# Kernel optimization log

Hardware: AMD Instinct MI355X
Metric: run time of the kernel (lower is better)

Reference implementation:

```python
import jax, jax.numpy as jnp
import numpy as np


def setup_inputs() -> dict:
    key = jax.random.key(0)
    k1, k2 = jax.random.split(key)
    inputs = jax.random.normal(k1, (16, 4096, 512), dtype=jnp.float32)
    # torch init is uniform(-1/num_codes, 1/num_codes); match scale
    codebooks = jax.random.uniform(k2, (4, 1024, 512), dtype=jnp.float32,
                                   minval=-1.0 / 1024, maxval=1.0 / 1024)
    return {"inputs": inputs, "codebooks": codebooks}


def _vq_level(flat, codebook):
    # flat: [N, D], codebook: [K, D]
    dists = (jnp.sum(flat * flat, axis=1, keepdims=True)
             + jnp.sum(codebook * codebook, axis=1)
             - 2.0 * jnp.matmul(flat, codebook.T))  # [N, K]
    idx = jnp.argmin(dists, axis=1)                  # [N]
    quantized = codebook[idx]                         # [N, D]
    return quantized, idx


def reference(inputs, codebooks):
    sg = jax.lax.stop_gradient
    num_levels = codebooks.shape[0]
    shp = inputs.shape
    D = shp[-1]
    flat_in = inputs.reshape(-1, D)

    residual = flat_in
    total_q = jnp.zeros_like(flat_in)
    all_idx = []
    total_q_loss = jnp.float32(0.0)
    total_e_loss = jnp.float32(0.0)
    for lvl in range(num_levels):
        quantized, idx = _vq_level(residual, codebooks[lvl])
        q_loss = jnp.mean((quantized - sg(residual)) ** 2)
        e_loss = jnp.mean((sg(quantized) - residual) ** 2)
        all_idx.append(idx.reshape(shp[:-1]))
        total_q = total_q + quantized
        total_q_loss = total_q_loss + q_loss
        total_e_loss = total_e_loss + e_loss
        residual = residual - sg(quantized)

    total_q = total_q.reshape(shp)
    final_ste = inputs + sg(total_q - inputs)
    return (final_ste,
            total_q_loss / num_levels,
            total_e_loss / num_levels,
            jnp.stack(all_idx, axis=0))
```

## Files before the change

### kernel.cpp

```cpp
#include <hip/hip_runtime.h>


#define NROWS 65536
#define DDIM  512
#define KC    1024

#define AS1 __attribute__((address_space(1)))
#define AS3 __attribute__((address_space(3)))

typedef __attribute__((ext_vector_type(8))) short short8v;
typedef __attribute__((ext_vector_type(4))) float f32x4;

__device__ __forceinline__ unsigned short f2bf(float f) {
  unsigned u = __float_as_uint(f);
  unsigned r = (u + 0x7FFFu + ((u >> 16) & 1u)) >> 16;
  return (unsigned short)r;
}

__device__ __forceinline__ bool lexlt(float v1, int i1, float v2, int i2) {
  return (v1 < v2) || (v1 == v2 && i1 < i2);
}

__device__ __forceinline__ void merge3(float& v0, float& v1, float& v2,
                                       float m0, float m1, float m2) {
  float x1 = fmaxf(v0, m0); v0 = fminf(v0, m0);
  float y = fminf(v1, m1), z = fmaxf(v1, m1);
  float nv1 = fminf(x1, y);
  v2 = fminf(fmaxf(x1, y), fminf(z, fminf(v2, m2)));
  v1 = nv1;
}

__device__ __forceinline__ void top3of4(float k0, float k1, float k2, float k3,
                                        float& m0, float& m1, float& m2) {
  float a = fminf(k0, k1), b = fmaxf(k0, k1);
  float c = fminf(k2, k3), d = fmaxf(k2, k3);
  m0 = fminf(a, c);
  float f = fmaxf(a, c), g = fminf(b, d);
  m1 = fminf(f, g); m2 = fmaxf(f, g);
}

__device__ __forceinline__ void wg_barrier() {
  asm volatile("" ::: "memory");
  __builtin_amdgcn_s_barrier();
  asm volatile("" ::: "memory");
}


__global__ void cnorm_kernel(const float* __restrict__ cbs,
                             float* __restrict__ cn32) {
  const int code = blockIdx.x;
  const int l = threadIdx.x;
  if (l >= 32) return;
  const int b = l >> 3, j = l & 7;
  const float* p = cbs + (size_t)code * DDIM + b * 128 + j;
  float racc;
  {
    #pragma clang fp contract(off)
    float x0 = p[0];
    racc = x0 * x0;
    for (int s = 1; s < 16; ++s) { float x = p[8 * s]; float sq = x * x; racc = racc + sq; }
  }
  {
    #pragma clang fp contract(off)
    float o;
    o = __shfl_xor(racc, 1, 64);  racc = racc + o;
    o = __shfl_xor(racc, 2, 64);  racc = racc + o;
    o = __shfl_xor(racc, 4, 64);  racc = racc + o;
    o = __shfl_xor(racc, 8, 64);  racc = racc + o;
    o = __shfl_xor(racc, 16, 64); racc = racc + o;
    if (l == 0) cn32[code] = racc;
  }
}

__global__ void cvt_bf16_kernel(const float4* __restrict__ in4,
                                ushort4* __restrict__ o4, long n4) {
  for (long i = blockIdx.x * (long)blockDim.x + threadIdx.x; i < n4;
       i += (long)gridDim.x * blockDim.x) {
    float4 v = in4[i];
    ushort4 o; o.x = f2bf(v.x); o.y = f2bf(v.y); o.z = f2bf(v.z); o.w = f2bf(v.w);
    o4[i] = o;
  }
}

__global__ void __launch_bounds__(256)
resupd_kernel(const float4* __restrict__ x4, const float* __restrict__ cbs,
              const float* __restrict__ idx_f, ushort4* __restrict__ res4,
              int nlev) {
  const int gwave = (blockIdx.x * 256 + threadIdx.x) >> 6;
  const int lane  = threadIdx.x & 63;
  const int nwaves = gridDim.x * 4;
  const float4* cb4 = (const float4*)cbs;
  for (int row = gwave; row < NROWS; row += nwaves) {
    int ci[4];
    for (int l = 0; l < nlev; ++l) ci[l] = (int)idx_f[(size_t)l * NROWS + row];
    #pragma unroll
    for (int half = 0; half < 2; ++half) {
      const int p = half * 64 + lane;
      float4 v = x4[(size_t)row * 128 + p];
      for (int l = 0; l < nlev; ++l) {
        const float4 c = cb4[((size_t)(l * KC + ci[l])) * 128 + p];
        v.x -= c.x; v.y -= c.y; v.z -= c.z; v.w -= c.w;
      }
      ushort4 o; o.x = f2bf(v.x); o.y = f2bf(v.y); o.z = f2bf(v.z); o.w = f2bf(v.w);
      res4[(size_t)row * 128 + p] = o;
    }
  }
}

template <int LVL>
__global__ void __launch_bounds__(256, 4)
score_gemm(const ushort* __restrict__ res, const ushort* __restrict__ cbb,
           const float* __restrict__ cn32, float* __restrict__ partials) {
  __shared__ ushort At[2][128 * 32];
  __shared__ ushort Bt[2][128 * 32];
  __shared__ float halfTop[2][2][64][3];

  const int t = threadIdx.x;
  const int w = t >> 6, lane = t & 63;
  const int fr = lane & 15, kg = lane >> 4;
  const int rh = w >> 1, ch = w & 1;
  const int xcd = blockIdx.x & 7;
  const int j   = blockIdx.x >> 3;
  const int colTile = j & 7;
  const int rowTile = xcd * 64 + (j >> 3);
  const int row0 = rowTile * 128;

  const ushort* Asrc = res + (size_t)row0 * DDIM;
  const ushort* Bsrc = cbb + ((size_t)LVL * KC + colTile * 128) * DDIM;

  const int r0s = t >> 2, kq = t & 3;
  const int r1s = 64 + r0s;
  const int swz = (t >> 3) & 3;
  const size_t off0 = (size_t)r0s * DDIM + (size_t)((kq ^ swz) * 8);
  const size_t off1 = (size_t)r1s * DDIM + (size_t)((kq ^ swz) * 8);
  const int kgs = (kg ^ ((fr >> 1) & 3)) * 8;

  f32x4 acc[4][4];
  #pragma unroll
  for (int ri = 0; ri < 4; ++ri)
    #pragma unroll
    for (int ci = 0; ci < 4; ++ci) { f32x4 z = {0.f, 0.f, 0.f, 0.f}; acc[ri][ci] = z; }

#define STG(KS, BI)                                                           \
  do {                                                                        \
    __builtin_amdgcn_global_load_lds(                                         \
        (const AS1 unsigned*)(Asrc + off0 + (KS) * 32),                       \
        (AS3 unsigned*)&At[BI][w * 512], 16, 0, 0);                           \
    __builtin_amdgcn_global_load_lds(                                         \
        (const AS1 unsigned*)(Asrc + off1 + (KS) * 32),                       \
        (AS3 unsigned*)&At[BI][2048 + w * 512], 16, 0, 0);                    \
    __builtin_amdgcn_global_load_lds(                                         \
        (const AS1 unsigned*)(Bsrc + off0 + (KS) * 32),                       \
        (AS3 unsigned*)&Bt[BI][w * 512], 16, 0, 0);                           \
    __builtin_amdgcn_global_load_lds(                                         \
        (const AS1 unsigned*)(Bsrc + off1 + (KS) * 32),                       \
        (AS3 unsigned*)&Bt[BI][2048 + w * 512], 16, 0, 0);                    \
  } while (0)

  STG(0, 0);
  #pragma unroll
  for (int ks = 0; ks < 16; ++ks) {
    const int cur = ks & 1;
    if (ks < 15) {
      STG(ks + 1, !cur);
      asm volatile("s_waitcnt vmcnt(4)" ::: "memory");
    } else {
      asm volatile("s_waitcnt vmcnt(0)" ::: "memory");
    }
    wg_barrier();
    short8v a[4], b[4];
    #pragma unroll
    for (int i = 0; i < 4; ++i)
      a[i] = *(const short8v*)&At[cur][(rh * 64 + i * 16 + fr) * 32 + kgs];
    #pragma unroll
    for (int i = 0; i < 4; ++i)
      b[i] = *(const short8v*)&Bt[cur][(ch * 64 + i * 16 + fr) * 32 + kgs];
    __builtin_amdgcn_s_setprio(1);
    #pragma unroll
    for (int ri = 0; ri < 4; ++ri)
      #pragma unroll
      for (int ci = 0; ci < 4; ++ci)
        acc[ri][ci] = __builtin_amdgcn_mfma_f32_16x16x32_bf16(
            a[ri], b[ci], acc[ri][ci], 0, 0, 0);
    __builtin_amdgcn_s_setprio(0);
    wg_barrier();
  }
#undef STG

  float cnv[4];
  #pragma unroll
  for (int ci = 0; ci < 4; ++ci)
    cnv[ci] = cn32[LVL * KC + colTile * 128 + ch * 64 + ci * 16 + fr] + 0.25f;

  #pragma unroll
  for (int ri = 0; ri < 4; ++ri) {
    #pragma unroll
    for (int j2 = 0; j2 < 4; ++j2) {
      float k[4];
      #pragma unroll
      for (int ci = 0; ci < 4; ++ci) {
        float s = fmaf(-2.0f, acc[ri][ci][j2], cnv[ci]);
        unsigned col = (unsigned)(colTile * 128 + ch * 64 + ci * 16 + fr);
        unsigned u = (__float_as_uint(s) & 0xFFFFFC00u) | col;
        k[ci] = __uint_as_float(u);
      }
      float m0, m1, m2;
      top3of4(k[0], k[1], k[2], k[3], m0, m1, m2);
      #pragma unroll
      for (int m = 1; m <= 8; m <<= 1) {
        float t0 = __shfl_xor(m0, m, 64);
        float t1 = __shfl_xor(m1, m, 64);
        float t2 = __shfl_xor(m2, m, 64);
        merge3(m0, m1, m2, t0, t1, t2);
      }
      if (fr == 0) {
        int row64 = ri * 16 + kg * 4 + j2;
        halfTop[rh][ch][row64][0] = m0;
        halfTop[rh][ch][row64][1] = m1;
        halfTop[rh][ch][row64][2] = m2;
      }
    }
  }
  __syncthreads();

  if (t < 128) {
    const int lrh = t >> 6, r64 = t & 63;
    float u0 = halfTop[lrh][0][r64][0], u1 = halfTop[lrh][0][r64][1],
          u2 = halfTop[lrh][0][r64][2];
    float s0 = halfTop[lrh][1][r64][0], s1 = halfTop[lrh][1][r64][1],
          s2 = halfTop[lrh][1][r64][2];
    merge3(u0, u1, u2, s0, s1, s2);
    const int grow = row0 + lrh * 64 + r64;
    partials[(size_t)(colTile * 3 + 0) * NROWS + grow] = u0;
    partials[(size_t)(colTile * 3 + 1) * NROWS + grow] = u1;
    partials[(size_t)(colTile * 3 + 2) * NROWS + grow] = u2;
  }
}

__global__ void __launch_bounds__(256)
combine_kernel(const float* __restrict__ partials, float* __restrict__ idx_io,
               int* __restrict__ qcnt, int* __restrict__ qrows,
               int* __restrict__ qcand, int LVL) {
  const int row = blockIdx.x * 256 + threadIdx.x;
  float v0 = 3.4e38f, v1 = 3.4e38f, v2 = 3.4e38f, v3 = 3.4e38f;
  #pragma unroll
  for (int p = 0; p < 24; ++p) {
    const float kv = partials[(size_t)p * NROWS + row];
    const bool b3 = kv < v3, b2 = kv < v2, b1 = kv < v1, b0 = kv < v0;
    v3 = b3 ? (b2 ? v2 : kv) : v3;
    v2 = b2 ? (b1 ? v1 : kv) : v2;
    v1 = b1 ? (b0 ? v0 : kv) : v1;
    v0 = b0 ? kv : v0;
  }
  if (v1 - v0 > 1e-3f) {
    idx_io[(size_t)LVL * NROWS + row] = (float)(__float_as_uint(v0) & 1023u);
  } else {
    int pos = atomicAdd(qcnt, 1);
    qrows[pos] = row;
    qcand[pos * 4 + 0] = (int)(__float_as_uint(v0) & 1023u);
    qcand[pos * 4 + 1] = (int)(__float_as_uint(v1) & 1023u);
    qcand[pos * 4 + 2] = (int)(__float_as_uint(v2) & 1023u);
    qcand[pos * 4 + 3] = (int)(__float_as_uint(v3) & 1023u);
  }
}

template <int LVL>
__global__ void __launch_bounds__(256)
refine_kernel(const float* __restrict__ x, const float* __restrict__ cbs,
              const float* __restrict__ cn32, float* __restrict__ idx_io,
              const int* __restrict__ qcnt, const int* __restrict__ qrows,
              const int* __restrict__ qcand) {
  const int qn = *qcnt;
  const float4* x4  = (const float4*)x;
  const float4* cb4 = (const float4*)cbs;
  const float*  cnL = cn32 + LVL * KC;

  for (int wi = blockIdx.x * 256 + threadIdx.x; wi < qn * 4;
       wi += gridDim.x * 256) {
    const int qi = wi >> 2, cd = wi & 3;
    const int grow = qrows[qi];
    const int ci   = qcand[qi * 4 + cd];
    const float4* xr = x4 + (size_t)grow * 128;
    const float4* cq = cb4 + ((size_t)LVL * KC + ci) * 128;
    const float4* cl[LVL > 0 ? LVL : 1];
    #pragma unroll
    for (int l = 0; l < LVL; ++l)
      cl[l] = cb4 +
              ((size_t)(l * KC + (int)idx_io[(size_t)l * NROWS + grow])) * 128;

    float Bk[4];
    float dacc = 0.0f;
    #pragma unroll
    for (int b = 0; b < 4; ++b) {
      #pragma clang fp contract(off)
      float racc[8];
      for (int s = 0; s < 16; ++s) {
        const int q = b * 32 + s * 2;
        float4 v0 = xr[q], v1 = xr[q + 1];
        #pragma unroll
        for (int l = 0; l < LVL; ++l) {
          const float4 c0 = cl[l][q], c1 = cl[l][q + 1];
          v0.x -= c0.x; v0.y -= c0.y; v0.z -= c0.z; v0.w -= c0.w;
          v1.x -= c1.x; v1.y -= c1.y; v1.z -= c1.z; v1.w -= c1.w;
        }
        if (s == 0) {
          racc[0] = v0.x * v0.x; racc[1] = v0.y * v0.y;
          racc[2] = v0.z * v0.z; racc[3] = v0.w * v0.w;
          racc[4] = v1.x * v1.x; racc[5] = v1.y * v1.y;
          racc[6] = v1.z * v1.z; racc[7] = v1.w * v1.w;
        } else {
          float sq;
          sq = v0.x * v0.x; racc[0] = racc[0] + sq;
          sq = v0.y * v0.y; racc[1] = racc[1] + sq;
          sq = v0.z * v0.z; racc[2] = racc[2] + sq;
          sq = v0.w * v0.w; racc[3] = racc[3] + sq;
          sq = v1.x * v1.x; racc[4] = racc[4] + sq;
          sq = v1.y * v1.y; racc[5] = racc[5] + sq;
          sq = v1.z * v1.z; racc[6] = racc[6] + sq;
          sq = v1.w * v1.w; racc[7] = racc[7] + sq;
        }
        const float4 c0 = cq[q], c1 = cq[q + 1];
        dacc = fmaf(v0.x, c0.x, dacc); dacc = fmaf(v0.y, c0.y, dacc);
        dacc = fmaf(v0.z, c0.z, dacc); dacc = fmaf(v0.w, c0.w, dacc);
        dacc = fmaf(v1.x, c1.x, dacc); dacc = fmaf(v1.y, c1.y, dacc);
        dacc = fmaf(v1.z, c1.z, dacc); dacc = fmaf(v1.w, c1.w, dacc);
      }
      float t0 = (racc[0] + racc[1]) + (racc[2] + racc[3]);
      float t1 = (racc[4] + racc[5]) + (racc[6] + racc[7]);
      Bk[b] = t0 + t1;
    }
    float vfin;
    {
      #pragma clang fp contract(off)
      float Arow = (Bk[0] + Bk[1]) + (Bk[2] + Bk[3]);
      float ab = Arow + cnL[ci];
      vfin = ab - 2.0f * dacc;
    }
    float bv = vfin; int bi = ci;
    float ov = __shfl_xor(bv, 1, 64); int oi = __shfl_xor(bi, 1, 64);
    if (lexlt(ov, oi, bv, bi)) { bv = ov; bi = oi; }
    ov = __shfl_xor(bv, 2, 64); oi = __shfl_xor(bi, 2, 64);
    if (lexlt(ov, oi, bv, bi)) { bv = ov; bi = oi; }
    if (cd == 0) idx_io[(size_t)LVL * NROWS + grow] = (float)bi;
  }
}

__global__ void __launch_bounds__(256)
finalize_kernel(const float4* __restrict__ x4, const float* __restrict__ cbs,
                const float* __restrict__ idx_f, float4* __restrict__ out,
                double* __restrict__ loss_acc) {
  double ls0 = 0.0, ls1 = 0.0, ls2 = 0.0, ls3 = 0.0;
  const int gwave = (blockIdx.x * 256 + threadIdx.x) >> 6;
  const int lane  = threadIdx.x & 63;
  const int nwaves = gridDim.x * 4;
  const float4* cb4 = (const float4*)cbs;

  for (int row = gwave; row < NROWS; row += nwaves) {
    int ci[4];
    #pragma unroll
    for (int l = 0; l < 4; ++l) ci[l] = (int)idx_f[(size_t)l * NROWS + row];
    #pragma unroll
    for (int half = 0; half < 2; ++half) {
      const int p = half * 64 + lane;
      const float4 xv = x4[(size_t)row * 128 + p];
      float4 rr = xv;
      float4 tq = make_float4(0.f, 0.f, 0.f, 0.f);
      #pragma unroll
      for (int l = 0; l < 4; ++l) {
        const float4 qv = cb4[((size_t)(l * KC + ci[l])) * 128 + p];
        rr.x -= qv.x; rr.y -= qv.y; rr.z -= qv.z; rr.w -= qv.w;
        const double ss = (double)rr.x * rr.x + (double)rr.y * rr.y +
                          (double)rr.z * rr.z + (double)rr.w * rr.w;
        if      (l == 0) ls0 += ss;
        else if (l == 1) ls1 += ss;
        else if (l == 2) ls2 += ss;
        else             ls3 += ss;
        tq.x += qv.x; tq.y += qv.y; tq.z += qv.z; tq.w += qv.w;
      }
      float4 o;
      o.x = xv.x + (tq.x - xv.x);
      o.y = xv.y + (tq.y - xv.y);
      o.z = xv.z + (tq.z - xv.z);
      o.w = xv.w + (tq.w - xv.w);
      out[(size_t)row * 128 + p] = o;
    }
  }
  #pragma unroll
  for (int m = 1; m <= 32; m <<= 1) {
    ls0 += __shfl_xor(ls0, m, 64);
    ls1 += __shfl_xor(ls1, m, 64);
    ls2 += __shfl_xor(ls2, m, 64);
    ls3 += __shfl_xor(ls3, m, 64);
  }
  __shared__ double sred[4][4];
  const int wave = threadIdx.x >> 6;
  if ((threadIdx.x & 63) == 0) {
    sred[wave][0] = ls0; sred[wave][1] = ls1; sred[wave][2] = ls2; sred[wave][3] = ls3;
  }
  __syncthreads();
  if (threadIdx.x < 4) {
    const double v = sred[0][threadIdx.x] + sred[1][threadIdx.x] +
                     sred[2][threadIdx.x] + sred[3][threadIdx.x];
    atomicAdd(loss_acc + threadIdx.x, v);
  }
}

__global__ void write_losses_kernel(const double* __restrict__ loss_acc,
                                    float* __restrict__ out) {
  if (threadIdx.x == 0 && blockIdx.x == 0) {
    const double inv = 1.0 / (double)((size_t)NROWS * (size_t)DDIM);
    const double tv = (loss_acc[0] * inv + loss_acc[1] * inv +
                       loss_acc[2] * inv + loss_acc[3] * inv) * 0.25;
    out[33554432] = (float)tv;
    out[33554433] = (float)tv;
  }
}

extern "C" void kernel_launch(void* const* d_in, const int* in_sizes, int n_in,
                              void* d_out, int out_size, void* d_ws, size_t ws_size,
                              hipStream_t stream) {
  (void)in_sizes; (void)n_in; (void)out_size; (void)ws_size;
  const float* x   = (const float*)d_in[0];
  const float* cbs = (const float*)d_in[1];
  float* out_f     = (float*)d_out;
  float* idx_f     = out_f + 33554434;

  ushort* cbb  = (ushort*)d_ws;
  ushort* res  = (ushort*)((char*)d_ws + 4194304);
  float*  cn32 = (float*)((char*)d_ws + 4194304 + 67108864);
  double* loss = (double*)((char*)d_ws + 4194304 + 67108864 + 16384);

  float* partials = out_f;
  int*   qcnt  = (int*)(out_f + 1572864);
  int*   qrows = (int*)(out_f + 1572868);
  int*   qcand = (int*)(out_f + 1638404);

  hipMemsetAsync(loss, 0, 4 * sizeof(double), stream);
  hipMemsetAsync(qcnt, 0, 4 * sizeof(int), stream);

  cnorm_kernel<<<4096, 64, 0, stream>>>(cbs, cn32);
  cvt_bf16_kernel<<<2048, 256, 0, stream>>>((const float4*)cbs, (ushort4*)cbb,
                                            (long)4 * KC * DDIM / 4);
  resupd_kernel<<<2048, 256, 0, stream>>>((const float4*)x, cbs, idx_f,
                                          (ushort4*)res, 0);

  score_gemm<0><<<4096, 256, 0, stream>>>(res, cbb, cn32, partials);
  combine_kernel<<<256, 256, 0, stream>>>(partials, idx_f, qcnt + 0, qrows, qcand, 0);
  refine_kernel<0><<<1024, 256, 0, stream>>>(x, cbs, cn32, idx_f, qcnt + 0, qrows, qcand);
  resupd_kernel<<<2048, 256, 0, stream>>>((const float4*)x, cbs, idx_f,
                                          (ushort4*)res, 1);

  score_gemm<1><<<4096, 256, 0, stream>>>(res, cbb, cn32, partials);
  combine_kernel<<<256, 256, 0, stream>>>(partials, idx_f, qcnt + 1, qrows, qcand, 1);
  refine_kernel<1><<<1024, 256, 0, stream>>>(x, cbs, cn32, idx_f, qcnt + 1, qrows, qcand);
  resupd_kernel<<<2048, 256, 0, stream>>>((const float4*)x, cbs, idx_f,
                                          (ushort4*)res, 2);

  score_gemm<2><<<4096, 256, 0, stream>>>(res, cbb, cn32, partials);
  combine_kernel<<<256, 256, 0, stream>>>(partials, idx_f, qcnt + 2, qrows, qcand, 2);
  refine_kernel<2><<<1024, 256, 0, stream>>>(x, cbs, cn32, idx_f, qcnt + 2, qrows, qcand);
  resupd_kernel<<<2048, 256, 0, stream>>>((const float4*)x, cbs, idx_f,
                                          (ushort4*)res, 3);

  score_gemm<3><<<4096, 256, 0, stream>>>(res, cbb, cn32, partials);
  combine_kernel<<<256, 256, 0, stream>>>(partials, idx_f, qcnt + 3, qrows, qcand, 3);
  refine_kernel<3><<<1024, 256, 0, stream>>>(x, cbs, cn32, idx_f, qcnt + 3, qrows, qcand);

  finalize_kernel<<<2048, 256, 0, stream>>>((const float4*)x, cbs, idx_f,
                                            (float4*)d_out, loss);
  write_losses_kernel<<<1, 64, 0, stream>>>(loss, out_f);
}
```

Before: 960.3 us.

## Refine all rows exactly and fuse residual update into refine kernel

The per-level resupd kernel is removed. Its bf16 residual write now happens at the end of refine_kernel, which already has the input row and the chosen codebook rows on hand, so a separate full pass over x is avoided. The margin-based shortcut and the atomic compaction queue in combine are also dropped. Every row now gets an exact fp32 rescoring of its top-4 candidates, which removes the atomics and the queue bookkeeping but multiplies the refine work per level. Each thread also streams a whole row on its own, so the memory accesses are strided and poorly coalesced.

Result: slower. 1.727 ms (+79.8%).

```diff
diff --git a/kernel.cpp b/kernel.cpp
--- a/kernel.cpp
+++ b/kernel.cpp
@@ -238,9 +238,8 @@
 }
 
 __global__ void __launch_bounds__(256)
-combine_kernel(const float* __restrict__ partials, float* __restrict__ idx_io,
-               int* __restrict__ qcnt, int* __restrict__ qrows,
-               int* __restrict__ qcand, int LVL) {
+combine_kernel(const float* __restrict__ partials, int* __restrict__ qcand,
+               int LVL) {
   const int row = blockIdx.x * 256 + threadIdx.x;
   float v0 = 3.4e38f, v1 = 3.4e38f, v2 = 3.4e38f, v3 = 3.4e38f;
   #pragma unroll
@@ -252,34 +251,25 @@
     v1 = b1 ? (b0 ? v0 : kv) : v1;
     v0 = b0 ? kv : v0;
   }
-  if (v1 - v0 > 1e-3f) {
-    idx_io[(size_t)LVL * NROWS + row] = (float)(__float_as_uint(v0) & 1023u);
-  } else {
-    int pos = atomicAdd(qcnt, 1);
-    qrows[pos] = row;
-    qcand[pos * 4 + 0] = (int)(__float_as_uint(v0) & 1023u);
-    qcand[pos * 4 + 1] = (int)(__float_as_uint(v1) & 1023u);
-    qcand[pos * 4 + 2] = (int)(__float_as_uint(v2) & 1023u);
-    qcand[pos * 4 + 3] = (int)(__float_as_uint(v3) & 1023u);
-  }
+  qcand[row * 4 + 0] = (int)(__float_as_uint(v0) & 1023u);
+  qcand[row * 4 + 1] = (int)(__float_as_uint(v1) & 1023u);
+  qcand[row * 4 + 2] = (int)(__float_as_uint(v2) & 1023u);
+  qcand[row * 4 + 3] = (int)(__float_as_uint(v3) & 1023u);
 }
 
 template <int LVL>
 __global__ void __launch_bounds__(256)
 refine_kernel(const float* __restrict__ x, const float* __restrict__ cbs,
               const float* __restrict__ cn32, float* __restrict__ idx_io,
-              const int* __restrict__ qcnt, const int* __restrict__ qrows,
-              const int* __restrict__ qcand) {
-  const int qn = *qcnt;
+              const int* __restrict__ qcand, ushort4* __restrict__ res4) {
   const float4* x4  = (const float4*)x;
   const float4* cb4 = (const float4*)cbs;
   const float*  cnL = cn32 + LVL * KC;
 
-  for (int wi = blockIdx.x * 256 + threadIdx.x; wi < qn * 4;
+  for (int wi = blockIdx.x * 256 + threadIdx.x; wi < NROWS * 4;
        wi += gridDim.x * 256) {
-    const int qi = wi >> 2, cd = wi & 3;
-    const int grow = qrows[qi];
-    const int ci   = qcand[qi * 4 + cd];
+    const int grow = wi >> 2, cd = wi & 3;
+    const int ci   = qcand[grow * 4 + cd];
     const float4* xr = x4 + (size_t)grow * 128;
     const float4* cq = cb4 + ((size_t)LVL * KC + ci) * 128;
     const float4* cl[LVL > 0 ? LVL : 1];
@@ -342,6 +332,24 @@
     ov = __shfl_xor(bv, 2, 64); oi = __shfl_xor(bi, 2, 64);
     if (lexlt(ov, oi, bv, bi)) { bv = ov; bi = oi; }
     if (cd == 0) idx_io[(size_t)LVL * NROWS + grow] = (float)bi;
+
+    if constexpr (LVL < 3) {
+      const float4* cbn = cb4 + ((size_t)(LVL * KC + bi)) * 128;
+      #pragma unroll 4
+      for (int q = cd * 32; q < cd * 32 + 32; ++q) {
+        float4 v = xr[q];
+        #pragma unroll
+        for (int l = 0; l < LVL; ++l) {
+          const float4 c = cl[l][q];
+          v.x -= c.x; v.y -= c.y; v.z -= c.z; v.w -= c.w;
+        }
+        const float4 c = cbn[q];
+        v.x -= c.x; v.y -= c.y; v.z -= c.z; v.w -= c.w;
+        ushort4 o;
+        o.x = f2bf(v.x); o.y = f2bf(v.y); o.z = f2bf(v.z); o.w = f2bf(v.w);
+        res4[(size_t)grow * 128 + q] = o;
+      }
+    }
   }
 }
 
@@ -431,12 +439,9 @@
   double* loss = (double*)((char*)d_ws + 4194304 + 67108864 + 16384);
 
   float* partials = out_f;
-  int*   qcnt  = (int*)(out_f + 1572864);
-  int*   qrows = (int*)(out_f + 1572868);
-  int*   qcand = (int*)(out_f + 1638404);
+  int*   qcand    = (int*)(out_f + 1572864);
 
   hipMemsetAsync(loss, 0, 4 * sizeof(double), stream);
-  hipMemsetAsync(qcnt, 0, 4 * sizeof(int), stream);
 
   cnorm_kernel<<<4096, 64, 0, stream>>>(cbs, cn32);
   cvt_bf16_kernel<<<2048, 256, 0, stream>>>((const float4*)cbs, (ushort4*)cbb,
@@ -445,26 +450,24 @@
                                           (ushort4*)res, 0);
 
   score_gemm<0><<<4096, 256, 0, stream>>>(res, cbb, cn32, partials);
-  combine_kernel<<<256, 256, 0, stream>>>(partials, idx_f, qcnt + 0, qrows, qcand, 0);
-  refine_kernel<0><<<1024, 256, 0, stream>>>(x, cbs, cn32, idx_f, qcnt + 0, qrows, qcand);
-  resupd_kernel<<<2048, 256, 0, stream>>>((const float4*)x, cbs, idx_f,
-                                          (ushort4*)res, 1);
+  combine_kernel<<<256, 256, 0, stream>>>(partials, qcand, 0);
+  refine_kernel<0><<<1024, 256, 0, stream>>>(x, cbs, cn32, idx_f, qcand,
+                                             (ushort4*)res);
 
   score_gemm<1><<<4096, 256, 0, stream>>>(res, cbb, cn32, partials);
-  combine_kernel<<<256, 256, 0, stream>>>(partials, idx_f, qcnt + 1, qrows, qcand, 1);
-  refine_kernel<1><<<1024, 256, 0, stream>>>(x, cbs, cn32, idx_f, qcnt + 1, qrows, qcand);
-  resupd_kernel<<<2048, 256, 0, stream>>>((const float4*)x, cbs, idx_f,
-                                          (ushort4*)res, 2);
+  combine_kernel<<<256, 256, 0, stream>>>(partials, qcand, 1);
+  refine_kernel<1><<<1024, 256, 0, stream>>>(x, cbs, cn32, idx_f, qcand,
+                                             (ushort4*)res);
 
   score_gemm<2><<<4096, 256, 0, stream>>>(res, cbb, cn32, partials);
-  combine_kernel<<<256, 256, 0, stream>>>(partials, idx_f, qcnt + 2, qrows, qcand, 2);
-  refine_kernel<2><<<1024, 256, 0, stream>>>(x, cbs, cn32, idx_f, qcnt + 2, qrows, qcand);
-  resupd_kernel<<<2048, 256, 0, stream>>>((const float4*)x, cbs, idx_f,
-                                          (ushort4*)res, 3);
+  combine_kernel<<<256, 256, 0, stream>>>(partials, qcand, 2);
+  refine_kernel<2><<<1024, 256, 0, stream>>>(x, cbs, cn32, idx_f, qcand,
+                                             (ushort4*)res);
 
   score_gemm<3><<<4096, 256, 0, stream>>>(res, cbb, cn32, partials);
-  combine_kernel<<<256, 256, 0, stream>>>(partials, idx_f, qcnt + 3, qrows, qcand, 3);
-  refine_kernel<3><<<1024, 256, 0, stream>>>(x, cbs, cn32, idx_f, qcnt + 3, qrows, qcand);
+  combine_kernel<<<256, 256, 0, stream>>>(partials, qcand, 3);
+  refine_kernel<3><<<1024, 256, 0, stream>>>(x, cbs, cn32, idx_f, qcand,
+                                             (ushort4*)res);
 
   finalize_kernel<<<2048, 256, 0, stream>>>((const float4*)x, cbs, idx_f,
                                             (float4*)d_out, loss);
```

## Fuse prep kernels and alias score_gemm LDS to fit five blocks per CU

Applied to the files above, without the earlier changes.

Merges codebook-norm, codebook bf16 conversion and the initial input-to-bf16 residual conversion into one prep kernel, removing two launches. In score_gemm, the epilogue top-3 scratch now reuses the GEMM staging buffer instead of its own shared array, cutting LDS per block so launch bounds can ask for 5 blocks per CU. The tighter register budget from the higher occupancy target may cause spills in the 16-accumulator MFMA loop.

After: 2.045 ms. 2.13x slower.

```diff
diff --git a/kernel.cpp b/kernel.cpp
--- a/kernel.cpp
+++ b/kernel.cpp
@@ -45,40 +45,45 @@
   asm volatile("" ::: "memory");
 }
 
-
-__global__ void cnorm_kernel(const float* __restrict__ cbs,
-                             float* __restrict__ cn32) {
+__global__ void __launch_bounds__(256)
+prep_kernel(const float* __restrict__ cbs, float* __restrict__ cn32,
+            const float4* __restrict__ x4, ushort4* __restrict__ cbb4,
+            ushort4* __restrict__ res4) {
   const int code = blockIdx.x;
   const int l = threadIdx.x;
-  if (l >= 32) return;
-  const int b = l >> 3, j = l & 7;
-  const float* p = cbs + (size_t)code * DDIM + b * 128 + j;
-  float racc;
-  {
-    #pragma clang fp contract(off)
-    float x0 = p[0];
-    racc = x0 * x0;
-    for (int s = 1; s < 16; ++s) { float x = p[8 * s]; float sq = x * x; racc = racc + sq; }
-  }
-  {
-    #pragma clang fp contract(off)
-    float o;
-    o = __shfl_xor(racc, 1, 64);  racc = racc + o;
-    o = __shfl_xor(racc, 2, 64);  racc = racc + o;
-    o = __shfl_xor(racc, 4, 64);  racc = racc + o;
-    o = __shfl_xor(racc, 8, 64);  racc = racc + o;
-    o = __shfl_xor(racc, 16, 64); racc = racc + o;
-    if (l == 0) cn32[code] = racc;
-  }
-}
-
-__global__ void cvt_bf16_kernel(const float4* __restrict__ in4,
-                                ushort4* __restrict__ o4, long n4) {
-  for (long i = blockIdx.x * (long)blockDim.x + threadIdx.x; i < n4;
-       i += (long)gridDim.x * blockDim.x) {
-    float4 v = in4[i];
+  if (l < 32) {
+    const int b = l >> 3, j = l & 7;
+    const float* p = cbs + (size_t)code * DDIM + b * 128 + j;
+    float racc;
+    {
+      #pragma clang fp contract(off)
+      float x0 = p[0];
+      racc = x0 * x0;
+      for (int s = 1; s < 16; ++s) { float x = p[8 * s]; float sq = x * x; racc = racc + sq; }
+    }
+    {
+      #pragma clang fp contract(off)
+      float o;
+      o = __shfl_xor(racc, 1, 64);  racc = racc + o;
+      o = __shfl_xor(racc, 2, 64);  racc = racc + o;
+      o = __shfl_xor(racc, 4, 64);  racc = racc + o;
+      o = __shfl_xor(racc, 8, 64);  racc = racc + o;
+      o = __shfl_xor(racc, 16, 64); racc = racc + o;
+      if (l == 0) cn32[code] = racc;
+    }
+  }
+  const float4* cb4 = (const float4*)cbs;
+  for (long i = blockIdx.x * 256L + threadIdx.x; i < 524288L;
+       i += (long)gridDim.x * 256) {
+    float4 v = cb4[i];
     ushort4 o; o.x = f2bf(v.x); o.y = f2bf(v.y); o.z = f2bf(v.z); o.w = f2bf(v.w);
-    o4[i] = o;
+    cbb4[i] = o;
+  }
+  for (long i = blockIdx.x * 256L + threadIdx.x; i < 8388608L;
+       i += (long)gridDim.x * 256) {
+    float4 v = x4[i];
+    ushort4 o; o.x = f2bf(v.x); o.y = f2bf(v.y); o.z = f2bf(v.z); o.w = f2bf(v.w);
+    res4[i] = o;
   }
 }
 
@@ -108,12 +113,10 @@
 }
 
 template <int LVL>
-__global__ void __launch_bounds__(256, 4)
+__global__ void __launch_bounds__(256, 5)
 score_gemm(const ushort* __restrict__ res, const ushort* __restrict__ cbb,
            const float* __restrict__ cn32, float* __restrict__ partials) {
-  __shared__ ushort At[2][128 * 32];
-  __shared__ ushort Bt[2][128 * 32];
-  __shared__ float halfTop[2][2][64][3];
+  __shared__ ushort lds[16384];
 
   const int t = threadIdx.x;
   const int w = t >> 6, lane = t & 63;
@@ -145,16 +148,16 @@
   do {                                                                        \
     __builtin_amdgcn_global_load_lds(                                         \
         (const AS1 unsigned*)(Asrc + off0 + (KS) * 32),                       \
-        (AS3 unsigned*)&At[BI][w * 512], 16, 0, 0);                           \
+        (AS3 unsigned*)&lds[(BI) * 4096 + w * 512], 16, 0, 0);                \
     __builtin_amdgcn_global_load_lds(                                         \
         (const AS1 unsigned*)(Asrc + off1 + (KS) * 32),                       \
-        (AS3 unsigned*)&At[BI][2048 + w * 512], 16, 0, 0);                    \
+        (AS3 unsigned*)&lds[(BI) * 4096 + 2048 + w * 512], 16, 0, 0);         \
     __builtin_amdgcn_global_load_lds(                                         \
         (const AS1 unsigned*)(Bsrc + off0 + (KS) * 32),                       \
-        (AS3 unsigned*)&Bt[BI][w * 512], 16, 0, 0);                           \
+        (AS3 unsigned*)&lds[8192 + (BI) * 4096 + w * 512], 16, 0, 0);         \
     __builtin_amdgcn_global_load_lds(                                         \
         (const AS1 unsigned*)(Bsrc + off1 + (KS) * 32),                       \
-        (AS3 unsigned*)&Bt[BI][2048 + w * 512], 16, 0, 0);                    \
+        (AS3 unsigned*)&lds[8192 + (BI) * 4096 + 2048 + w * 512], 16, 0, 0);  \
   } while (0)
 
   STG(0, 0);
@@ -171,10 +174,10 @@
     short8v a[4], b[4];
     #pragma unroll
     for (int i = 0; i < 4; ++i)
-      a[i] = *(const short8v*)&At[cur][(rh * 64 + i * 16 + fr) * 32 + kgs];
+      a[i] = *(const short8v*)&lds[cur * 4096 + (rh * 64 + i * 16 + fr) * 32 + kgs];
     #pragma unroll
     for (int i = 0; i < 4; ++i)
-      b[i] = *(const short8v*)&Bt[cur][(ch * 64 + i * 16 + fr) * 32 + kgs];
+      b[i] = *(const short8v*)&lds[8192 + cur * 4096 + (ch * 64 + i * 16 + fr) * 32 + kgs];
     __builtin_amdgcn_s_setprio(1);
     #pragma unroll
     for (int ri = 0; ri < 4; ++ri)
@@ -187,6 +190,7 @@
   }
 #undef STG
 
+  float* hT = (float*)lds;
   float cnv[4];
   #pragma unroll
   for (int ci = 0; ci < 4; ++ci)
@@ -215,9 +219,9 @@
       }
       if (fr == 0) {
         int row64 = ri * 16 + kg * 4 + j2;
-        halfTop[rh][ch][row64][0] = m0;
-        halfTop[rh][ch][row64][1] = m1;
-        halfTop[rh][ch][row64][2] = m2;
+        hT[(((rh * 2 + ch) * 64) + row64) * 3 + 0] = m0;
+        hT[(((rh * 2 + ch) * 64) + row64) * 3 + 1] = m1;
+        hT[(((rh * 2 + ch) * 64) + row64) * 3 + 2] = m2;
       }
     }
   }
@@ -225,10 +229,12 @@
 
   if (t < 128) {
     const int lrh = t >> 6, r64 = t & 63;
-    float u0 = halfTop[lrh][0][r64][0], u1 = halfTop[lrh][0][r64][1],
-          u2 = halfTop[lrh][0][r64][2];
-    float s0 = halfTop[lrh][1][r64][0], s1 = halfTop[lrh][1][r64][1],
-          s2 = halfTop[lrh][1][r64][2];
+    float u0 = hT[(((lrh * 2 + 0) * 64) + r64) * 3 + 0];
+    float u1 = hT[(((lrh * 2 + 0) * 64) + r64) * 3 + 1];
+    float u2 = hT[(((lrh * 2 + 0) * 64) + r64) * 3 + 2];
+    float s0 = hT[(((lrh * 2 + 1) * 64) + r64) * 3 + 0];
+    float s1 = hT[(((lrh * 2 + 1) * 64) + r64) * 3 + 1];
+    float s2 = hT[(((lrh * 2 + 1) * 64) + r64) * 3 + 2];
     merge3(u0, u1, u2, s0, s1, s2);
     const int grow = row0 + lrh * 64 + r64;
     partials[(size_t)(colTile * 3 + 0) * NROWS + grow] = u0;
@@ -438,11 +444,8 @@
   hipMemsetAsync(loss, 0, 4 * sizeof(double), stream);
   hipMemsetAsync(qcnt, 0, 4 * sizeof(int), stream);
 
-  cnorm_kernel<<<4096, 64, 0, stream>>>(cbs, cn32);
-  cvt_bf16_kernel<<<2048, 256, 0, stream>>>((const float4*)cbs, (ushort4*)cbb,
-                                            (long)4 * KC * DDIM / 4);
-  resupd_kernel<<<2048, 256, 0, stream>>>((const float4*)x, cbs, idx_f,
-                                          (ushort4*)res, 0);
+  prep_kernel<<<4096, 256, 0, stream>>>(cbs, cn32, (const float4*)x,
+                                        (ushort4*)cbb, (ushort4*)res);
 
   score_gemm<0><<<4096, 256, 0, stream>>>(res, cbb, cn32, partials);
   combine_kernel<<<256, 256, 0, stream>>>(partials, idx_f, qcnt + 0, qrows, qcand, 0);
```
